# Kernel optimization log

Measured on AMD Instinct MI355X. Metric: run time of the kernel, lower is better.

## Reference

```python
import jax, jax.numpy as jnp
import numpy as np

# dims: C=d_model, DI=expand*C (d_inner), S=d_state, R=dt_rank, K=4 scan dirs
C, DI, S, R, K = 64, 128, 16, 4, 4
Hh, Ww, T, Bsz = 48, 48, 4, 1

def _silu(x):
    return x * jax.nn.sigmoid(x)

def _ln_c(x, w, b, eps=1e-6):
    # LayerNorm2d: normalize over channel dim of [B,C,H,W]
    mu = jnp.mean(x, axis=1, keepdims=True)
    var = jnp.var(x, axis=1, keepdims=True)
    return (x - mu) * jax.lax.rsqrt(var + eps) * w[None, :, None, None] + b[None, :, None, None]

def _cal_kl(cur, prev):
    # elementwise KL over channel-softmax distributions, shape-preserving
    lp = jax.nn.log_softmax(prev, axis=1)
    lq = jax.nn.log_softmax(cur, axis=1)
    return jnp.exp(lp) * (lp - lq)

def _ss2d(x, in_w, in_b, cw, cb, xp_w, dt_w, dt_b, A_logs, Ds, onw, onb, ow, ob):
    # VMamba-style SS2D, channel-first input [B,C,H,W]
    B_, _, H_, W_ = x.shape
    L = H_ * W_
    xz = jnp.einsum('dc,bchw->bdhw', in_w, x) + in_b[None, :, None, None]
    xc, z = jnp.split(xz, 2, axis=1)
    di = xc.shape[1]
    xc = jax.lax.conv_general_dilated(xc, cw[:, None], (1, 1), 'SAME',
        dimension_numbers=('NCHW', 'OIHW', 'NCHW'), feature_group_count=di)
    xc = _silu(xc + cb[None, :, None, None])
    # cross-scan: row-major, col-major, and their reverses -> [B,K,DI,L]
    x1 = xc.reshape(B_, di, L)
    x2 = jnp.swapaxes(xc, 2, 3).reshape(B_, di, L)
    xs = jnp.stack([x1, x2, jnp.flip(x1, -1), jnp.flip(x2, -1)], axis=1)
    xdbl = jnp.einsum('krd,bkdl->bkrl', xp_w, xs)
    dts, Bs, Cs = jnp.split(xdbl, [R, R + S], axis=2)  # [B,K,R,L],[B,K,S,L],[B,K,S,L]
    dt = jax.nn.softplus(jnp.einsum('kdr,bkrl->bkdl', dt_w, dts) + dt_b[None, :, :, None])
    A = -jnp.exp(A_logs)  # [K,DI,S]
    dA = jnp.exp(dt[..., None] * A[None, :, :, None, :])                    # [B,K,DI,L,S]
    dBx = (dt * xs)[..., None] * jnp.swapaxes(Bs, 2, 3)[:, :, None, :, :]   # [B,K,DI,L,S]
    def comb(e1, e2):
        a1, b1 = e1
        a2, b2 = e2
        return (a1 * a2, a2 * b1 + b2)
    _, hs = jax.lax.associative_scan(comb, (dA, dBx), axis=3)
    y = jnp.einsum('bkdls,bksl->bkdl', hs, Cs) + Ds[None, :, :, None] * xs
    # cross-merge back to row-major and sum
    y0 = y[:, 0]
    y1 = jnp.swapaxes(y[:, 1].reshape(B_, di, W_, H_), 2, 3).reshape(B_, di, L)
    y2 = jnp.flip(y[:, 2], -1)
    y3 = jnp.swapaxes(jnp.flip(y[:, 3], -1).reshape(B_, di, W_, H_), 2, 3).reshape(B_, di, L)
    yy = (y0 + y1 + y2 + y3).reshape(B_, di, H_, W_)
    yy = _ln_c(yy, onw, onb) * _silu(z)
    return jnp.einsum('cd,bdhw->bchw', ow, yy) + ob[None, :, None, None]

def setup_inputs():
    key = jax.random.key(0)
    ks = jax.random.split(key, 16)
    rn = lambda k, shp, s: jax.random.normal(k, shp, jnp.float32) * s
    return {
        'image_sequence': rn(ks[0], (Bsz, T, C, Hh, Ww), 1.0),
        'difficult_zone': rn(ks[1], (Bsz, C, Hh, Ww), 1.0),
        'sigma': rn(ks[2], (Bsz, C, Hh, Ww), 0.1),
        # params stacked over the 2 SS2D modules: [0]=mamba_sigma, [1]=mamba_bias
        'in_w': rn(ks[3], (2, 2 * DI, C), C ** -0.5),
        'in_b': rn(ks[4], (2, 2 * DI), 0.02),
        'conv_w': rn(ks[5], (2, DI, 3, 3), 1.0 / 3.0),
        'conv_b': rn(ks[6], (2, DI), 0.02),
        'xp_w': rn(ks[7], (2, K, R + 2 * S, DI), DI ** -0.5),
        'dt_w': rn(ks[8], (2, K, DI, R), R ** -0.5),
        'dt_b': rn(ks[9], (2, K, DI), 0.5),
        'A_logs': jnp.log(1.0 + jax.random.uniform(ks[10], (2, K, DI, S), jnp.float32)),
        'Ds': rn(ks[11], (2, K, DI), 0.5),
        'onw': jnp.ones((2, DI), jnp.float32),
        'onb': jnp.zeros((2, DI), jnp.float32),
        'ow': rn(ks[12], (2, C, DI), 0.02),
        'ob': jnp.zeros((2, C), jnp.float32),
        'niw': jnp.ones((C,), jnp.float32),
        'nib': jnp.zeros((C,), jnp.float32),
        'ndw': jnp.ones((C,), jnp.float32),
        'ndb': jnp.zeros((C,), jnp.float32),
    }

def reference(image_sequence, difficult_zone, sigma, in_w, in_b, conv_w, conv_b, xp_w, dt_w, dt_b, A_logs, Ds, onw, onb, ow, ob, niw, nib, ndw, ndb):
    prev = _ln_c(difficult_zone, ndw, ndb)
    cur = prev * jnp.exp(sigma)  # prev / exp(-sigma)
    for t in range(T):  # strictly sequential recurrence over `length` steps
        s = _ss2d(_cal_kl(cur, prev), in_w[0], in_b[0], conv_w[0], conv_b[0], xp_w[0],
                  dt_w[0], dt_b[0], A_logs[0], Ds[0], onw[0], onb[0], ow[0], ob[0])
        bias = _ss2d(_ln_c(image_sequence[:, t], niw, nib), in_w[1], in_b[1], conv_w[1], conv_b[1], xp_w[1],
                     dt_w[1], dt_b[1], A_logs[1], Ds[1], onw[1], onb[1], ow[1], ob[1])
        cur, prev = cur * jnp.exp(s) + bias, cur
    return cur
```

## Files before the change

kernel.cpp:

```cpp
#include <hip/hip_runtime.h>

#define DEV __device__ __forceinline__

constexpr int Cc = 64, DIc = 128, Sc = 16, Rc = 4, Kc = 4;
constexpr int Lc = 2304, Tc = 4;
constexpr int NCH = 144, CHL = 16;

constexpr int OFF_XCPRE = 0;
constexpr int OFF_Z     = 294912;
constexpr int OFF_XACT  = 589824;
constexpr int OFF_DTS   = 884736;
constexpr int OFF_BS    = 921600;
constexpr int OFF_CS    = 1069056;
constexpr int OFF_Y     = 1216512;
constexpr int OFF_SUMA  = 2396160;
constexpr int OFF_SUMB  = 3575808;
constexpr int OFF_H0    = 4755456;
constexpr int SLOTF     = 5935104;
constexpr int OFF_B1    = 5 * SLOTF;
constexpr int OFF_B2    = OFF_B1 + Lc * Cc;
constexpr int OFF_BIAS  = OFF_B2 + Lc * Cc;
constexpr int OFF_TW    = OFF_BIAS + Tc * Lc * Cc;
constexpr int TW_INW  = 0;
constexpr int TW_XPW  = 32768;
constexpr int TW_OW   = 69632;
constexpr int TW_CW   = 86016;
constexpr int TW_AT   = 88320;
constexpr int TW_DTW  = 104704;

struct Params {
  const float *img, *dz, *sigma, *in_w, *in_b, *conv_w, *conv_b, *xp_w, *dt_w,
              *dt_b, *A_logs, *Ds, *onw, *onb, *ow, *ob, *niw, *nib, *ndw, *ndb;
  float* outp;
  float* ws;
};

DEV float wsum(float v) {
#pragma unroll
  for (int m = 32; m; m >>= 1) v += __shfl_xor(v, m, 64);
  return v;
}
DEV float wmax(float v) {
#pragma unroll
  for (int m = 32; m; m >>= 1) v = fmaxf(v, __shfl_xor(v, m, 64));
  return v;
}
DEV float sigmoidf(float x) { return 1.f / (1.f + __expf(-x)); }
DEV float softplusf(float v) { return (v > 20.f) ? v : __logf(1.f + __expf(v)); }

DEV int perm_idx(int k, int l) {
  if (k == 0) return l;
  if (k == 1) return (l % 48) * 48 + l / 48;
  if (k == 2) return Lc - 1 - l;
  int pp = Lc - 1 - l;
  return (pp % 48) * 48 + pp / 48;
}

__global__ __launch_bounds__(256) void g_transpose(Params p) {
  float* tw = p.ws + OFF_TW;
  int i = blockIdx.x * 256 + threadIdx.x;
  if (i < 32768) {
    int d = i & 255, cc = (i >> 8) & 63, b = i >> 14;
    tw[TW_INW + i] = p.in_w[(b * 256 + d) * 64 + cc];
  }
  if (i < 36864) {
    int kr = i % 144, cc = (i / 144) & 127, b = i / (144 * 128);
    tw[TW_XPW + i] = p.xp_w[(b * 144 + kr) * 128 + cc];
  }
  if (i < 16384) {
    int c = i & 63, d = (i >> 6) & 127, b = i >> 13;
    tw[TW_OW + i] = p.ow[(b * 64 + c) * 128 + d];
  }
  if (i < 2304) {
    int d = i & 127, kk = (i >> 7) % 9, b = i / 1152;
    tw[TW_CW + i] = p.conv_w[(b * 128 + d) * 9 + kk];
  }
  if (i < 16384) {
    int d = i & 127, bks = i >> 7;
    int s = bks & 15, bk = bks >> 4;
    tw[TW_AT + i] = p.A_logs[(bk * 128 + d) * 16 + s];
  }
  if (i < 4096) {
    int d = i & 127, bkr = i >> 7;
    int r = bkr & 3, bk = bkr >> 2;
    tw[TW_DTW + i] = p.dt_w[(bk * 128 + d) * 4 + r];
  }
}

__global__ __launch_bounds__(256) void g_inproj(Params p) {
  __shared__ float xv[8][64];
  int tid = threadIdx.x;
  int slot = blockIdx.y;
  int branch = (slot >= 4) ? 0 : 1;
  float* ws = p.ws;
  float* base = ws + (size_t)slot * SLOTF;
  float* xcpre = base + OFF_XCPRE;
  float* zbuf  = base + OFF_Z;
  const float* wT = ws + OFF_TW + TW_INW + branch * 64 * 256;
  int l0 = blockIdx.x * 8;
  int wv = tid >> 6, c = tid & 63;
#pragma unroll
  for (int q = 0; q < 2; q++) {
    int pp = wv * 2 + q;
    int l = l0 + pp;
    float x;
    if (branch == 1) {
      float v = p.img[(slot * Cc + c) * Lc + l];
      float mu = wsum(v) * (1.f / 64.f);
      float var = wsum(v * v) * (1.f / 64.f) - mu * mu;
      x = (v - mu) * rsqrtf(var + 1e-6f) * p.niw[c] + p.nib[c];
    } else {
      float v = p.dz[c * Lc + l];
      float mu = wsum(v) * (1.f / 64.f);
      float var = wsum(v * v) * (1.f / 64.f) - mu * mu;
      float pv = (v - mu) * rsqrtf(var + 1e-6f) * p.ndw[c] + p.ndb[c];
      float cv = pv * __expf(p.sigma[c * Lc + l]);
      (ws + OFF_B1)[l * Cc + c] = cv;
      float mp = wmax(pv);
      float sp = wsum(__expf(pv - mp));
      float lp = pv - mp - __logf(sp);
      float mq = wmax(cv);
      float sq = wsum(__expf(cv - mq));
      float lq = cv - mq - __logf(sq);
      x = __expf(lp) * (lp - lq);
    }
    xv[pp][c] = x;
  }
  __syncthreads();
  int d = tid;
  float acc[8];
#pragma unroll
  for (int q = 0; q < 8; q++) acc[q] = 0.f;
  for (int cc = 0; cc < Cc; cc++) {
    float wval = wT[cc * 256 + d];
#pragma unroll
    for (int q = 0; q < 8; q++) acc[q] += wval * xv[q][cc];
  }
  float bv = p.in_b[branch * 2 * DIc + d];
  if (d < DIc) {
#pragma unroll
    for (int q = 0; q < 8; q++) xcpre[(l0 + q) * DIc + d] = acc[q] + bv;
  } else {
    int dd = d - DIc;
#pragma unroll
    for (int q = 0; q < 8; q++) zbuf[(l0 + q) * DIc + dd] = acc[q] + bv;
  }
}

__global__ __launch_bounds__(256) void g_conv(Params p, int slot_base) {
  __shared__ float xv[4][DIc];
  int tid = threadIdx.x;
  int slot = slot_base + blockIdx.y;
  int branch = (slot >= 4) ? 0 : 1;
  float* ws = p.ws;
  float* base = ws + (size_t)slot * SLOTF;
  float* xcpre = base + OFF_XCPRE;
  float* xact  = base + OFF_XACT;
  float* dtsb  = base + OFF_DTS;
  float* Bsb   = base + OFF_BS;
  float* Csb   = base + OFF_CS;
  const float* cwT  = ws + OFF_TW + TW_CW + branch * 9 * 128;
  const float* xpwT = ws + OFF_TW + TW_XPW + branch * 128 * 144;
  int h = blockIdx.x / 12;
  int w0 = (blockIdx.x % 12) * 4;
  for (int it = tid; it < 4 * DIc; it += 256) {
    int d = it & (DIc - 1);
    int pp = it >> 7;
    int w = w0 + pp;
    float acc = 0.f;
#pragma unroll
    for (int kh = 0; kh < 3; kh++) {
      int hh = h + kh - 1;
      if ((unsigned)hh < 48u) {
#pragma unroll
        for (int kw = 0; kw < 3; kw++) {
          int wp = w + kw - 1;
          if ((unsigned)wp < 48u)
            acc += cwT[(kh * 3 + kw) * 128 + d] * xcpre[(hh * 48 + wp) * DIc + d];
        }
      }
    }
    float v = acc + p.conv_b[branch * DIc + d];
    float s = v * sigmoidf(v);
    xv[pp][d] = s;
    xact[(h * 48 + w) * DIc + d] = s;
  }
  __syncthreads();
  if (tid < Kc * 36) {
    int k = tid / 36, r = tid % 36;
    float acc[4] = {0.f, 0.f, 0.f, 0.f};
    for (int cc = 0; cc < DIc; cc++) {
      float wvv = xpwT[cc * 144 + tid];
#pragma unroll
      for (int pp = 0; pp < 4; pp++) acc[pp] += wvv * xv[pp][cc];
    }
#pragma unroll
    for (int pp = 0; pp < 4; pp++) {
      int w = w0 + pp;
      int lr = h * 48 + w, lcx = w * 48 + h;
      int pos = (k == 0) ? lr : (k == 1) ? lcx : (k == 2) ? (Lc - 1 - lr) : (Lc - 1 - lcx);
      if (r < Rc) dtsb[(k * Rc + r) * Lc + pos] = acc[pp];
      else if (r < Rc + Sc) Bsb[(k * Lc + pos) * Sc + (r - Rc)] = acc[pp];
      else Csb[(k * Lc + pos) * Sc + (r - Rc - Sc)] = acc[pp];
    }
  }
}

__global__ __launch_bounds__(256) void g_scan1(Params p, int slot_base) {
  int gid = blockIdx.x * 256 + threadIdx.x;
  int slot = slot_base + blockIdx.y;
  int branch = (slot >= 4) ? 0 : 1;
  float* ws = p.ws;
  float* base = ws + (size_t)slot * SLOTF;
  const float* xact = base + OFF_XACT;
  const float* Bsb  = base + OFF_BS;
  const float* dtsb = base + OFF_DTS;
  float* sumA = base + OFF_SUMA;
  float* sumB = base + OFF_SUMB;
  int d = gid & (DIc - 1);
  int k = (gid >> 7) & 3;
  int ch = gid >> 9;
  int bk = branch * Kc + k;
  const float* AT   = ws + OFF_TW + TW_AT;
  const float* dtwT = ws + OFF_TW + TW_DTW;
  float A[Sc];
#pragma unroll
  for (int s = 0; s < Sc; s++) A[s] = -__expf(AT[(bk * 16 + s) * 128 + d]);
  float dw[Rc];
#pragma unroll
  for (int r = 0; r < Rc; r++) dw[r] = dtwT[(bk * 4 + r) * 128 + d];
  float db = p.dt_b[bk * DIc + d];
  float pA[Sc], aB[Sc];
#pragma unroll
  for (int s = 0; s < Sc; s++) { pA[s] = 1.f; aB[s] = 0.f; }
  int l0 = ch * CHL;
  for (int i = 0; i < CHL; i++) {
    int l = l0 + i;
    float v = db;
#pragma unroll
    for (int r = 0; r < Rc; r++) v += dw[r] * dtsb[(k * Rc + r) * Lc + l];
    float dtv = softplusf(v);
    int idx = perm_idx(k, l);
    float xvv = xact[idx * DIc + d];
    float dtx = dtv * xvv;
    const float* Bf = Bsb + (k * Lc + l) * Sc;
#pragma unroll
    for (int s = 0; s < Sc; s++) {
      float da = __expf(dtv * A[s]);
      pA[s] *= da;
      aB[s] = da * aB[s] + dtx * Bf[s];
    }
  }
  float* sa = sumA + ((k * NCH + ch) * Sc) * DIc + d;
  float* sb = sumB + ((k * NCH + ch) * Sc) * DIc + d;
#pragma unroll
  for (int s = 0; s < Sc; s++) { sa[s * DIc] = pA[s]; sb[s * DIc] = aB[s]; }
}

__global__ __launch_bounds__(256) void g_mid(Params p, int slot_base) {
  int gid = blockIdx.x * 256 + threadIdx.x;
  int slot = slot_base + blockIdx.y;
  float* base = p.ws + (size_t)slot * SLOTF;
  const float* sumA = base + OFF_SUMA;
  const float* sumB = base + OFF_SUMB;
  float* h0 = base + OFF_H0;
  int d = gid & (DIc - 1);
  int s = (gid >> 7) & (Sc - 1);
  int k = gid >> 11;
  float h = 0.f;
  for (int g = 0; g < NCH / 16; g++) {
    float a[16], b[16];
#pragma unroll
    for (int j = 0; j < 16; j++) {
      int idx = ((k * NCH + g * 16 + j) * Sc + s) * DIc + d;
      a[j] = sumA[idx];
      b[j] = sumB[idx];
    }
#pragma unroll
    for (int j = 0; j < 16; j++) {
      int idx = ((k * NCH + g * 16 + j) * Sc + s) * DIc + d;
      h0[idx] = h;
      h = a[j] * h + b[j];
    }
  }
}

__global__ __launch_bounds__(256) void g_scan2(Params p, int slot_base) {
  int gid = blockIdx.x * 256 + threadIdx.x;
  int slot = slot_base + blockIdx.y;
  int branch = (slot >= 4) ? 0 : 1;
  float* ws = p.ws;
  float* base = ws + (size_t)slot * SLOTF;
  const float* xact = base + OFF_XACT;
  const float* Bsb  = base + OFF_BS;
  const float* Csb  = base + OFF_CS;
  const float* dtsb = base + OFF_DTS;
  const float* h0b  = base + OFF_H0;
  float* yb = base + OFF_Y;
  int d = gid & (DIc - 1);
  int k = (gid >> 7) & 3;
  int ch = gid >> 9;
  int bk = branch * Kc + k;
  const float* AT   = ws + OFF_TW + TW_AT;
  const float* dtwT = ws + OFF_TW + TW_DTW;
  float A[Sc];
#pragma unroll
  for (int s = 0; s < Sc; s++) A[s] = -__expf(AT[(bk * 16 + s) * 128 + d]);
  float dw[Rc];
#pragma unroll
  for (int r = 0; r < Rc; r++) dw[r] = dtwT[(bk * 4 + r) * 128 + d];
  float db = p.dt_b[bk * DIc + d];
  float h[Sc];
  const float* hp = h0b + ((k * NCH + ch) * Sc) * DIc + d;
#pragma unroll
  for (int s = 0; s < Sc; s++) h[s] = hp[s * DIc];
  float Dv = p.Ds[bk * DIc + d];
  int l0 = ch * CHL;
  for (int i = 0; i < CHL; i++) {
    int l = l0 + i;
    float v = db;
#pragma unroll
    for (int r = 0; r < Rc; r++) v += dw[r] * dtsb[(k * Rc + r) * Lc + l];
    float dtv = softplusf(v);
    int idx = perm_idx(k, l);
    float xvv = xact[idx * DIc + d];
    float dtx = dtv * xvv;
    const float* Bf = Bsb + (k * Lc + l) * Sc;
    const float* Cf = Csb + (k * Lc + l) * Sc;
    float acc = 0.f;
#pragma unroll
    for (int s = 0; s < Sc; s++) {
      float da = __expf(dtv * A[s]);
      h[s] = da * h[s] + dtx * Bf[s];
      acc += h[s] * Cf[s];
    }
    yb[(k * Lc + l) * DIc + d] = acc + Dv * xvv;
  }
}

__global__ __launch_bounds__(256) void g_out_bias(Params p) {
  __shared__ float yy[4][DIc];
  __shared__ float ml[4][DIc];
  __shared__ float mnv[4], isv[4];
  int tid = threadIdx.x;
  int slot = blockIdx.y;
  float* ws = p.ws;
  float* base = ws + (size_t)slot * SLOTF;
  const float* yb = base + OFF_Y;
  const float* zb = base + OFF_Z;
  const float* owT = ws + OFF_TW + TW_OW + 128 * 64;
  float* biasb = ws + OFF_BIAS;
  int l0 = blockIdx.x * 4;
  for (int it = tid; it < 4 * DIc; it += 256) {
    int d = it & (DIc - 1), pp = it >> 7;
    int l = l0 + pp;
    int www = l % 48, hh = l / 48;
    int lr = l, lcx = www * 48 + hh;
    float v = yb[(0 * Lc + lr) * DIc + d] + yb[(1 * Lc + lcx) * DIc + d] +
              yb[(2 * Lc + (Lc - 1 - lr)) * DIc + d] +
              yb[(3 * Lc + (Lc - 1 - lcx)) * DIc + d];
    yy[pp][d] = v;
  }
  __syncthreads();
  {
    int wv = tid >> 6, c = tid & 63;
    float a = yy[wv][c], b = yy[wv][c + 64];
    float s1 = wsum(a + b);
    float s2 = wsum(a * a + b * b);
    float mu = s1 * (1.f / 128.f);
    float var = s2 * (1.f / 128.f) - mu * mu;
    if (c == 0) { mnv[wv] = mu; isv[wv] = rsqrtf(var + 1e-6f); }
  }
  __syncthreads();
  for (int it = tid; it < 4 * DIc; it += 256) {
    int d = it & (DIc - 1), pp = it >> 7;
    int l = l0 + pp;
    float m = (yy[pp][d] - mnv[pp]) * isv[pp] * p.onw[DIc + d] + p.onb[DIc + d];
    float zv = zb[l * DIc + d];
    ml[pp][d] = m * zv * sigmoidf(zv);
  }
  __syncthreads();
  {
    int pp = tid >> 6, c = tid & 63;
    int l = l0 + pp;
    float acc = p.ob[Cc + c];
    for (int d2 = 0; d2 < DIc; d2++) acc += owT[d2 * 64 + c] * ml[pp][d2];
    biasb[(slot * Lc + l) * Cc + c] = acc;
  }
}

__global__ __launch_bounds__(256) void g_out_s(Params p, int targ, int fuse, int finalw,
                                               const float* curb, float* nxtb) {
  __shared__ float yy[4][DIc];
  __shared__ float ml[4][DIc];
  __shared__ float xvs[4][64];
  __shared__ float mnv[4], isv[4];
  int tid = threadIdx.x;
  float* ws = p.ws;
  float* base = ws + (size_t)4 * SLOTF;
  const float* yb = base + OFF_Y;
  const float* zb = base + OFF_Z;
  float* xcpre = base + OFF_XCPRE;
  float* zbuf  = base + OFF_Z;
  const float* owT  = ws + OFF_TW + TW_OW;
  const float* inwT = ws + OFF_TW + TW_INW;
  const float* biasb = ws + OFF_BIAS;
  int l0 = blockIdx.x * 4;
  for (int it = tid; it < 4 * DIc; it += 256) {
    int d = it & (DIc - 1), pp = it >> 7;
    int l = l0 + pp;
    int www = l % 48, hh = l / 48;
    int lr = l, lcx = www * 48 + hh;
    float v = yb[(0 * Lc + lr) * DIc + d] + yb[(1 * Lc + lcx) * DIc + d] +
              yb[(2 * Lc + (Lc - 1 - lr)) * DIc + d] +
              yb[(3 * Lc + (Lc - 1 - lcx)) * DIc + d];
    yy[pp][d] = v;
  }
  __syncthreads();
  {
    int wv = tid >> 6, c = tid & 63;
    float a = yy[wv][c], b = yy[wv][c + 64];
    float s1 = wsum(a + b);
    float s2 = wsum(a * a + b * b);
    float mu = s1 * (1.f / 128.f);
    float var = s2 * (1.f / 128.f) - mu * mu;
    if (c == 0) { mnv[wv] = mu; isv[wv] = rsqrtf(var + 1e-6f); }
  }
  __syncthreads();
  for (int it = tid; it < 4 * DIc; it += 256) {
    int d = it & (DIc - 1), pp = it >> 7;
    int l = l0 + pp;
    float m = (yy[pp][d] - mnv[pp]) * isv[pp] * p.onw[d] + p.onb[d];
    float zv = zb[l * DIc + d];
    ml[pp][d] = m * zv * sigmoidf(zv);
  }
  __syncthreads();
  {
    int pp = tid >> 6, c = tid & 63;
    int l = l0 + pp;
    float acc = p.ob[c];
    for (int d2 = 0; d2 < DIc; d2++) acc += owT[d2 * 64 + c] * ml[pp][d2];
    float cv = curb[l * Cc + c];
    float nv = cv * __expf(acc) + biasb[(targ * Lc + l) * Cc + c];
    nxtb[l * Cc + c] = nv;
    if (finalw) p.outp[c * Lc + l] = nv;
    if (fuse) {
      float mp = wmax(cv);
      float sp = wsum(__expf(cv - mp));
      float lp = cv - mp - __logf(sp);
      float mq = wmax(nv);
      float sq = wsum(__expf(nv - mq));
      float lq = nv - mq - __logf(sq);
      xvs[pp][c] = __expf(lp) * (lp - lq);
    }
  }
  if (fuse) {
    __syncthreads();
    int d = tid;
    float acc[4] = {0.f, 0.f, 0.f, 0.f};
    for (int cc = 0; cc < Cc; cc++) {
      float wval = inwT[cc * 256 + d];
#pragma unroll
      for (int pp = 0; pp < 4; pp++) acc[pp] += wval * xvs[pp][cc];
    }
    float bv = p.in_b[d];
    if (d < DIc) {
#pragma unroll
      for (int pp = 0; pp < 4; pp++) xcpre[(l0 + pp) * DIc + d] = acc[pp] + bv;
    } else {
      int dd = d - DIc;
#pragma unroll
      for (int pp = 0; pp < 4; pp++) zbuf[(l0 + pp) * DIc + dd] = acc[pp] + bv;
    }
  }
}

extern "C" void kernel_launch(void* const* d_in, const int* in_sizes, int n_in,
                              void* d_out, int out_size, void* d_ws, size_t ws_size,
                              hipStream_t stream) {
  (void)in_sizes; (void)n_in; (void)out_size; (void)ws_size;
  Params p;
  p.img    = (const float*)d_in[0];
  p.dz     = (const float*)d_in[1];
  p.sigma  = (const float*)d_in[2];
  p.in_w   = (const float*)d_in[3];
  p.in_b   = (const float*)d_in[4];
  p.conv_w = (const float*)d_in[5];
  p.conv_b = (const float*)d_in[6];
  p.xp_w   = (const float*)d_in[7];
  p.dt_w   = (const float*)d_in[8];
  p.dt_b   = (const float*)d_in[9];
  p.A_logs = (const float*)d_in[10];
  p.Ds     = (const float*)d_in[11];
  p.onw    = (const float*)d_in[12];
  p.onb    = (const float*)d_in[13];
  p.ow     = (const float*)d_in[14];
  p.ob     = (const float*)d_in[15];
  p.niw    = (const float*)d_in[16];
  p.nib    = (const float*)d_in[17];
  p.ndw    = (const float*)d_in[18];
  p.ndb    = (const float*)d_in[19];
  p.outp   = (float*)d_out;
  p.ws     = (float*)d_ws;


  hipLaunchKernelGGL(g_transpose, dim3(144), dim3(256), 0, stream, p);
  hipLaunchKernelGGL(g_inproj, dim3(288, 5), dim3(256), 0, stream, p);
  hipLaunchKernelGGL(g_conv, dim3(576, 5), dim3(256), 0, stream, p, 0);
  hipLaunchKernelGGL(g_scan1, dim3(288, 5), dim3(256), 0, stream, p, 0);
  hipLaunchKernelGGL(g_mid, dim3(32, 5), dim3(256), 0, stream, p, 0);
  hipLaunchKernelGGL(g_scan2, dim3(288, 5), dim3(256), 0, stream, p, 0);
  hipLaunchKernelGGL(g_out_bias, dim3(576, 4), dim3(256), 0, stream, p);

  float* b1 = p.ws + OFF_B1;
  float* b2 = p.ws + OFF_B2;
  hipLaunchKernelGGL(g_out_s, dim3(576), dim3(256), 0, stream, p, 0, 1, 0,
                     (const float*)b1, b2);
  for (int t = 1; t < Tc; t++) {
    const float* curb = (t & 1) ? b2 : b1;
    float* nxtb       = (t & 1) ? b1 : b2;
    hipLaunchKernelGGL(g_conv, dim3(576, 1), dim3(256), 0, stream, p, 4);
    hipLaunchKernelGGL(g_scan1, dim3(288, 1), dim3(256), 0, stream, p, 4);
    hipLaunchKernelGGL(g_mid, dim3(32, 1), dim3(256), 0, stream, p, 4);
    hipLaunchKernelGGL(g_scan2, dim3(288, 1), dim3(256), 0, stream, p, 4);
    hipLaunchKernelGGL(g_out_s, dim3(576), dim3(256), 0, stream, p,
                       t, (t == Tc - 1) ? 0 : 1, (t == Tc - 1) ? 1 : 0, curb, nxtb);
  }
}
```

Measured before the change: 436.6 us.

## Split scan state dimension across threads and stage dt/x chunk data in shared memory

Each scan block now handles one (direction, chunk) pair, with two thread halves each owning 8 of the 16 state dimensions. The softplus dt and dt*x values for the chunk are computed once cooperatively and stored in LDS, and B/C rows are staged in shared memory. The dts layout is changed to position-major so that a single float4 load fetches all four ranks. scan1 computes the chunk decay product in closed form as exp(A*sum(dt)) instead of multiplying it out step by step, and scan2 reduces the two halves' partial outputs through LDS. The aim is to double parallelism, lower register pressure, and cut redundant dt work and global loads, at the cost of extra syncs and reduction traffic.

New measurement: 403.2 us. 7.6% less time.

```diff
diff --git a/kernel.cpp b/kernel.cpp
--- a/kernel.cpp
+++ b/kernel.cpp
@@ -56,6 +56,10 @@
   return (pp % 48) * 48 + pp / 48;
 }
 
+DEV int perm_stride(int k) {
+  return (k == 0) ? 1 : (k == 1) ? 48 : (k == 2) ? -1 : -48;
+}
+
 __global__ __launch_bounds__(256) void g_transpose(Params p) {
   float* tw = p.ws + OFF_TW;
   int i = blockIdx.x * 256 + threadIdx.x;
@@ -199,7 +203,7 @@
       int w = w0 + pp;
       int lr = h * 48 + w, lcx = w * 48 + h;
       int pos = (k == 0) ? lr : (k == 1) ? lcx : (k == 2) ? (Lc - 1 - lr) : (Lc - 1 - lcx);
-      if (r < Rc) dtsb[(k * Rc + r) * Lc + pos] = acc[pp];
+      if (r < Rc) dtsb[(k * Lc + pos) * Rc + r] = acc[pp];
       else if (r < Rc + Sc) Bsb[(k * Lc + pos) * Sc + (r - Rc)] = acc[pp];
       else Csb[(k * Lc + pos) * Sc + (r - Rc - Sc)] = acc[pp];
     }
@@ -207,7 +211,11 @@
 }
 
 __global__ __launch_bounds__(256) void g_scan1(Params p, int slot_base) {
-  int gid = blockIdx.x * 256 + threadIdx.x;
+  __shared__ float sDtv[CHL][DIc];
+  __shared__ float sDtx[CHL][DIc];
+  __shared__ float sB[CHL * Sc];
+  __shared__ float sCT[2][DIc];
+  int tid = threadIdx.x;
   int slot = slot_base + blockIdx.y;
   int branch = (slot >= 4) ? 0 : 1;
   float* ws = p.ws;
@@ -217,44 +225,61 @@
   const float* dtsb = base + OFF_DTS;
   float* sumA = base + OFF_SUMA;
   float* sumB = base + OFF_SUMB;
-  int d = gid & (DIc - 1);
-  int k = (gid >> 7) & 3;
-  int ch = gid >> 9;
+  int bx = blockIdx.x;
+  int k = bx / NCH, ch = bx - k * NCH;
+  int d = tid & (DIc - 1);
+  int sh = tid >> 7;
   int bk = branch * Kc + k;
   const float* AT   = ws + OFF_TW + TW_AT;
   const float* dtwT = ws + OFF_TW + TW_DTW;
-  float A[Sc];
-#pragma unroll
-  for (int s = 0; s < Sc; s++) A[s] = -__expf(AT[(bk * 16 + s) * 128 + d]);
+  int l0 = ch * CHL;
+  sB[tid] = Bsb[(k * Lc + l0) * Sc + tid];
+  float A[8];
+#pragma unroll
+  for (int j = 0; j < 8; j++)
+    A[j] = -__expf(AT[(bk * 16 + sh * 8 + j) * 128 + d]);
   float dw[Rc];
 #pragma unroll
   for (int r = 0; r < Rc; r++) dw[r] = dtwT[(bk * 4 + r) * 128 + d];
   float db = p.dt_b[bk * DIc + d];
-  float pA[Sc], aB[Sc];
-#pragma unroll
-  for (int s = 0; s < Sc; s++) { pA[s] = 1.f; aB[s] = 0.f; }
-  int l0 = ch * CHL;
+  int idx0 = perm_idx(k, l0);
+  int st = perm_stride(k);
+  float ct = 0.f;
+#pragma unroll
+  for (int j = 0; j < 8; j++) {
+    int i = sh * 8 + j;
+    int l = l0 + i;
+    const float4 dt4 = *(const float4*)(dtsb + (size_t)(k * Lc + l) * 4);
+    float v = db + dw[0] * dt4.x + dw[1] * dt4.y + dw[2] * dt4.z + dw[3] * dt4.w;
+    float dtv = softplusf(v);
+    float xvv = xact[(idx0 + st * i) * DIc + d];
+    sDtv[i][d] = dtv;
+    sDtx[i][d] = dtv * xvv;
+    ct += dtv;
+  }
+  sCT[sh][d] = ct;
+  __syncthreads();
+  float CT = sCT[0][d] + sCT[1][d];
+  float h[8];
+#pragma unroll
+  for (int j = 0; j < 8; j++) h[j] = 0.f;
+#pragma unroll
   for (int i = 0; i < CHL; i++) {
-    int l = l0 + i;
-    float v = db;
-#pragma unroll
-    for (int r = 0; r < Rc; r++) v += dw[r] * dtsb[(k * Rc + r) * Lc + l];
-    float dtv = softplusf(v);
-    int idx = perm_idx(k, l);
-    float xvv = xact[idx * DIc + d];
-    float dtx = dtv * xvv;
-    const float* Bf = Bsb + (k * Lc + l) * Sc;
-#pragma unroll
-    for (int s = 0; s < Sc; s++) {
-      float da = __expf(dtv * A[s]);
-      pA[s] *= da;
-      aB[s] = da * aB[s] + dtx * Bf[s];
-    }
-  }
-  float* sa = sumA + ((k * NCH + ch) * Sc) * DIc + d;
-  float* sb = sumB + ((k * NCH + ch) * Sc) * DIc + d;
-#pragma unroll
-  for (int s = 0; s < Sc; s++) { sa[s * DIc] = pA[s]; sb[s * DIc] = aB[s]; }
+    float dtv = sDtv[i][d];
+    float dtx = sDtx[i][d];
+#pragma unroll
+    for (int j = 0; j < 8; j++) {
+      float da = __expf(dtv * A[j]);
+      h[j] = da * h[j] + dtx * sB[i * Sc + sh * 8 + j];
+    }
+  }
+  float* sa = sumA + ((size_t)(k * NCH + ch) * Sc + sh * 8) * DIc + d;
+  float* sb = sumB + ((size_t)(k * NCH + ch) * Sc + sh * 8) * DIc + d;
+#pragma unroll
+  for (int j = 0; j < 8; j++) {
+    sa[j * DIc] = __expf(A[j] * CT);
+    sb[j * DIc] = h[j];
+  }
 }
 
 __global__ __launch_bounds__(256) void g_mid(Params p, int slot_base) {
@@ -286,7 +311,11 @@
 }
 
 __global__ __launch_bounds__(256) void g_scan2(Params p, int slot_base) {
-  int gid = blockIdx.x * 256 + threadIdx.x;
+  __shared__ float sDtv[CHL][DIc];
+  __shared__ float sDtx[CHL][DIc];
+  __shared__ float sB[CHL * Sc];
+  __shared__ float sC[CHL * Sc];
+  int tid = threadIdx.x;
   int slot = slot_base + blockIdx.y;
   int branch = (slot >= 4) ? 0 : 1;
   float* ws = p.ws;
@@ -297,44 +326,76 @@
   const float* dtsb = base + OFF_DTS;
   const float* h0b  = base + OFF_H0;
   float* yb = base + OFF_Y;
-  int d = gid & (DIc - 1);
-  int k = (gid >> 7) & 3;
-  int ch = gid >> 9;
+  int bx = blockIdx.x;
+  int k = bx / NCH, ch = bx - k * NCH;
+  int d = tid & (DIc - 1);
+  int sh = tid >> 7;
   int bk = branch * Kc + k;
   const float* AT   = ws + OFF_TW + TW_AT;
   const float* dtwT = ws + OFF_TW + TW_DTW;
-  float A[Sc];
-#pragma unroll
-  for (int s = 0; s < Sc; s++) A[s] = -__expf(AT[(bk * 16 + s) * 128 + d]);
+  int l0 = ch * CHL;
+  sB[tid] = Bsb[(k * Lc + l0) * Sc + tid];
+  sC[tid] = Csb[(k * Lc + l0) * Sc + tid];
+  float A[8];
+#pragma unroll
+  for (int j = 0; j < 8; j++)
+    A[j] = -__expf(AT[(bk * 16 + sh * 8 + j) * 128 + d]);
   float dw[Rc];
 #pragma unroll
   for (int r = 0; r < Rc; r++) dw[r] = dtwT[(bk * 4 + r) * 128 + d];
   float db = p.dt_b[bk * DIc + d];
-  float h[Sc];
-  const float* hp = h0b + ((k * NCH + ch) * Sc) * DIc + d;
-#pragma unroll
-  for (int s = 0; s < Sc; s++) h[s] = hp[s * DIc];
   float Dv = p.Ds[bk * DIc + d];
-  int l0 = ch * CHL;
+  float h[8];
+  const float* hp = h0b + ((size_t)(k * NCH + ch) * Sc + sh * 8) * DIc + d;
+#pragma unroll
+  for (int j = 0; j < 8; j++) h[j] = hp[j * DIc];
+  int idx0 = perm_idx(k, l0);
+  int st = perm_stride(k);
+  float xs[8];
+#pragma unroll
+  for (int j = 0; j < 8; j++) {
+    int i = sh * 8 + j;
+    int l = l0 + i;
+    const float4 dt4 = *(const float4*)(dtsb + (size_t)(k * Lc + l) * 4);
+    float v = db + dw[0] * dt4.x + dw[1] * dt4.y + dw[2] * dt4.z + dw[3] * dt4.w;
+    float dtv = softplusf(v);
+    float xvv = xact[(idx0 + st * i) * DIc + d];
+    sDtv[i][d] = dtv;
+    sDtx[i][d] = dtv * xvv;
+    xs[j] = xvv;
+  }
+  __syncthreads();
+  float acc[CHL];
+#pragma unroll
   for (int i = 0; i < CHL; i++) {
-    int l = l0 + i;
-    float v = db;
-#pragma unroll
-    for (int r = 0; r < Rc; r++) v += dw[r] * dtsb[(k * Rc + r) * Lc + l];
-    float dtv = softplusf(v);
-    int idx = perm_idx(k, l);
-    float xvv = xact[idx * DIc + d];
-    float dtx = dtv * xvv;
-    const float* Bf = Bsb + (k * Lc + l) * Sc;
-    const float* Cf = Csb + (k * Lc + l) * Sc;
-    float acc = 0.f;
-#pragma unroll
-    for (int s = 0; s < Sc; s++) {
-      float da = __expf(dtv * A[s]);
-      h[s] = da * h[s] + dtx * Bf[s];
-      acc += h[s] * Cf[s];
-    }
-    yb[(k * Lc + l) * DIc + d] = acc + Dv * xvv;
+    float dtv = sDtv[i][d];
+    float dtx = sDtx[i][d];
+    float a = 0.f;
+#pragma unroll
+    for (int j = 0; j < 8; j++) {
+      float da = __expf(dtv * A[j]);
+      h[j] = da * h[j] + dtx * sB[i * Sc + sh * 8 + j];
+      a += h[j] * sC[i * Sc + sh * 8 + j];
+    }
+    acc[i] = a;
+  }
+  if (sh == 0) {
+#pragma unroll
+    for (int j = 0; j < 8; j++) acc[j] += Dv * xs[j];
+  } else {
+#pragma unroll
+    for (int j = 0; j < 8; j++) acc[8 + j] += Dv * xs[j];
+  }
+  __syncthreads();
+  if (sh == 1) {
+#pragma unroll
+    for (int i = 0; i < CHL; i++) sDtx[i][d] = acc[i];
+  }
+  __syncthreads();
+  if (sh == 0) {
+#pragma unroll
+    for (int i = 0; i < CHL; i++)
+      yb[(size_t)(k * Lc + l0 + i) * DIc + d] = acc[i] + sDtx[i][d];
   }
 }
 
@@ -507,9 +568,9 @@
   hipLaunchKernelGGL(g_transpose, dim3(144), dim3(256), 0, stream, p);
   hipLaunchKernelGGL(g_inproj, dim3(288, 5), dim3(256), 0, stream, p);
   hipLaunchKernelGGL(g_conv, dim3(576, 5), dim3(256), 0, stream, p, 0);
-  hipLaunchKernelGGL(g_scan1, dim3(288, 5), dim3(256), 0, stream, p, 0);
+  hipLaunchKernelGGL(g_scan1, dim3(Kc * NCH, 5), dim3(256), 0, stream, p, 0);
   hipLaunchKernelGGL(g_mid, dim3(32, 5), dim3(256), 0, stream, p, 0);
-  hipLaunchKernelGGL(g_scan2, dim3(288, 5), dim3(256), 0, stream, p, 0);
+  hipLaunchKernelGGL(g_scan2, dim3(Kc * NCH, 5), dim3(256), 0, stream, p, 0);
   hipLaunchKernelGGL(g_out_bias, dim3(576, 4), dim3(256), 0, stream, p);
 
   float* b1 = p.ws + OFF_B1;
@@ -520,9 +581,9 @@
     const float* curb = (t & 1) ? b2 : b1;
     float* nxtb       = (t & 1) ? b1 : b2;
     hipLaunchKernelGGL(g_conv, dim3(576, 1), dim3(256), 0, stream, p, 4);
-    hipLaunchKernelGGL(g_scan1, dim3(288, 1), dim3(256), 0, stream, p, 4);
+    hipLaunchKernelGGL(g_scan1, dim3(Kc * NCH, 1), dim3(256), 0, stream, p, 4);
     hipLaunchKernelGGL(g_mid, dim3(32, 1), dim3(256), 0, stream, p, 4);
-    hipLaunchKernelGGL(g_scan2, dim3(288, 1), dim3(256), 0, stream, p, 4);
+    hipLaunchKernelGGL(g_scan2, dim3(Kc * NCH, 1), dim3(256), 0, stream, p, 4);
     hipLaunchKernelGGL(g_out_s, dim3(576), dim3(256), 0, stream, p,
                        t, (t == Tc - 1) ? 0 : 1, (t == Tc - 1) ? 1 : 0, curb, nxtb);
   }
```
